# Kernel tuning notes

Measured on AMD Instinct MI355X. Metric: run time of the kernel, lower is better.

Reference implementation:

```python
import jax, jax.numpy as jnp
import numpy as np

B, N, D = 4, 2048, 512
H = 8
HD = D // H
MLP_H = 4 * D
SCALE = HD ** -0.5
ELEV_SCALE = 1000.0
EPS = 1e-5


def _ln(x, g, b):
    m = jnp.mean(x, axis=-1, keepdims=True)
    v = jnp.mean((x - m) ** 2, axis=-1, keepdims=True)
    return (x - m) * jax.lax.rsqrt(v + EPS) * g + b


def setup_inputs() -> dict:
    key = jax.random.key(0)
    ks = jax.random.split(key, 10)
    s = lambda fin: (2.0 / fin) ** 0.5
    return {
        "x": jax.random.normal(ks[0], (B, N, D), jnp.float32),
        "elevation_patches": jax.random.uniform(ks[1], (B, N), jnp.float32) * 3000.0,
        "ln1_g": jnp.ones((D,), jnp.float32),
        "ln1_b": jnp.zeros((D,), jnp.float32),
        "qkv_w": jax.random.normal(ks[2], (D, 3 * D), jnp.float32) * s(D),
        "alpha": jnp.ones((1,), jnp.float32),
        "proj_w": jax.random.normal(ks[3], (D, D), jnp.float32) * s(D),
        "proj_b": jnp.zeros((D,), jnp.float32),
        "ln2_g": jnp.ones((D,), jnp.float32),
        "ln2_b": jnp.zeros((D,), jnp.float32),
        "fc1_w": jax.random.normal(ks[4], (D, MLP_H), jnp.float32) * s(D),
        "fc1_b": jnp.zeros((MLP_H,), jnp.float32),
        "fc2_w": jax.random.normal(ks[5], (MLP_H, D), jnp.float32) * s(MLP_H),
        "fc2_b": jnp.zeros((D,), jnp.float32),
    }


def reference(x, elevation_patches, ln1_g, ln1_b, qkv_w, alpha, proj_w, proj_b,
              ln2_g, ln2_b, fc1_w, fc1_b, fc2_w, fc2_b):
    # --- attention ---
    h = _ln(x, ln1_g, ln1_b)
    qkv = (h @ qkv_w).reshape(B, N, 3, H, HD)
    q, k, v = (jnp.moveaxis(qkv[:, :, i], 1, 2) for i in range(3))  # [B,H,N,HD]
    scores = jnp.einsum('bhnd,bhmd->bhnm', q, k) * SCALE
    elev_diff = (elevation_patches[:, None, :] - elevation_patches[:, :, None]) / ELEV_SCALE
    bias = jnp.clip(-alpha[0] * jax.nn.relu(elev_diff), -10.0, 0.0)  # [B,N,N]
    attn = jax.nn.softmax(scores + bias[:, None], axis=-1)
    out = jnp.einsum('bhnm,bhmd->bhnd', attn, v)
    out = jnp.moveaxis(out, 1, 2).reshape(B, N, D) @ proj_w + proj_b
    x = x + out
    # --- mlp ---
    h2 = _ln(x, ln2_g, ln2_b)
    mlp = jax.nn.gelu(h2 @ fc1_w + fc1_b, approximate=False) @ fc2_w + fc2_b
    return x + mlp
```

## Files before the change

### kernel.cpp

```cpp
#include <hip/hip_runtime.h>
#include <math.h>

typedef unsigned short u16;
typedef unsigned int u32;

#define B_ 4
#define N_ 2048
#define D_ 512
#define H_ 8
#define HD_ 64
#define MLP_H_ 2048
#define EPS_ 1e-5f
#define C2_ 14.426950408889634f
#define QSCALE_ 0.1803368801111204f
#define EL2_ 0.0014426950408889634f

#if __has_builtin(__builtin_amdgcn_exp2f)
#define EXP2(x) __builtin_amdgcn_exp2f(x)
#else
#define EXP2(x) exp2f(x)
#endif
#if __has_builtin(__builtin_amdgcn_fmed3f)
#define CLAMP0C(x) __builtin_amdgcn_fmed3f((x), 0.0f, C2_)
#else
#define CLAMP0C(x) fminf(fmaxf((x), 0.0f), C2_)
#endif

__device__ __forceinline__ u16 bf16_rne(float x) {
  u32 u = __float_as_uint(x);
  u32 r = (u + 0x7FFFu + ((u >> 16) & 1u)) >> 16;
  return (u16)r;
}
#if __has_builtin(__builtin_amdgcn_cvt_pk_bf16_f32)
typedef __bf16 bf2_t __attribute__((ext_vector_type(2)));
__device__ __forceinline__ u32 pk_bf16(float a, float b) {
  bf2_t v = __builtin_amdgcn_cvt_pk_bf16_f32(a, b);
  u32 r; __builtin_memcpy(&r, &v, 4); return r;
}
#else
__device__ __forceinline__ u32 pk_bf16(float a, float b) {
  return (u32)bf16_rne(a) | ((u32)bf16_rne(b) << 16);
}
#endif
__device__ __forceinline__ void bf16_split(float x, u16& h, u16& l) {
  h = bf16_rne(x);
  float hf = __uint_as_float(((u32)h) << 16);
  l = bf16_rne(x - hf);
}

typedef __attribute__((ext_vector_type(8))) short bfrag;
typedef __attribute__((ext_vector_type(4))) float ffrag;

#define LDS_AS(p) ((__attribute__((address_space(3))) void*)(p))
#define GLB_AS(p) ((const __attribute__((address_space(1))) void*)(p))

__global__ __launch_bounds__(256) void ln_kernel(
    const float* __restrict__ x, const float* __restrict__ g,
    const float* __restrict__ b, u16* __restrict__ o,
    const float* __restrict__ elev, const float* __restrict__ alpha,
    float* __restrict__ e2)
{
  __shared__ float red[8];
  int row = blockIdx.x;
  int tid = threadIdx.x;
  if (e2 && tid == 0) e2[row] = elev[row] * (alpha[0] * EL2_);
  const float* xr = x + (size_t)row * D_;
  float v0 = xr[tid], v1 = xr[tid + 256];
  float s = v0 + v1;
  #pragma unroll
  for (int off = 32; off > 0; off >>= 1) s += __shfl_xor(s, off, 64);
  if ((tid & 63) == 0) red[tid >> 6] = s;
  __syncthreads();
  float mean = (red[0] + red[1] + red[2] + red[3]) * (1.0f / D_);
  float d0 = v0 - mean, d1 = v1 - mean;
  float vs = d0 * d0 + d1 * d1;
  #pragma unroll
  for (int off = 32; off > 0; off >>= 1) vs += __shfl_xor(vs, off, 64);
  if ((tid & 63) == 0) red[4 + (tid >> 6)] = vs;
  __syncthreads();
  float var = (red[4] + red[5] + red[6] + red[7]) * (1.0f / D_);
  float r = rsqrtf(var + EPS_);
  u16* orow = o + (size_t)row * D_;
  orow[tid]       = bf16_rne(d0 * r * g[tid] + b[tid]);
  orow[tid + 256] = bf16_rne(d1 * r * g[tid + 256] + b[tid + 256]);
}

__device__ __forceinline__ void wsplit_body(
    const float* __restrict__ W, u16* __restrict__ Thi, u16* __restrict__ Tlo,
    int K, int N, int bx, int by, int tid)
{
  __shared__ float tile[64][65];
  int n0 = bx * 64, k0 = by * 64;
  int c = tid & 63, r4 = tid >> 6;
  #pragma unroll
  for (int i = 0; i < 16; i++) {
    int r = r4 + i * 4;
    tile[r][c] = W[(size_t)(k0 + r) * N + n0 + c];
  }
  __syncthreads();
  #pragma unroll
  for (int i = 0; i < 16; i++) {
    int rn = r4 + i * 4;
    float v = tile[c][rn];
    size_t o = (size_t)(n0 + rn) * K + k0 + c;
    if (Tlo) {
      u16 h, l; bf16_split(v, h, l);
      Thi[o] = h; Tlo[o] = l;
    } else {
      Thi[o] = bf16_rne(v);
    }
  }
}

__global__ __launch_bounds__(256) void wsplit_all(
    const float* __restrict__ qkv_w, const float* __restrict__ proj_w,
    const float* __restrict__ fc1_w, const float* __restrict__ fc2_w,
    u16* __restrict__ qw_hi, u16* __restrict__ qw_lo,
    u16* __restrict__ pw_hi, u16* __restrict__ f1_hi, u16* __restrict__ f2_hi)
{
  int id = blockIdx.x;
  int tid = threadIdx.x;
  if (id < 192) {
    wsplit_body(qkv_w, qw_hi, qw_lo, 512, 1536, id % 24, id / 24, tid);
  } else if (id < 256) {
    int l = id - 192;
    wsplit_body(proj_w, pw_hi, nullptr, 512, 512, l % 8, l / 8, tid);
  } else if (id < 512) {
    int l = id - 256;
    wsplit_body(fc1_w, f1_hi, nullptr, 512, 2048, l % 32, l / 32, tid);
  } else {
    int l = id - 512;
    wsplit_body(fc2_w, f2_hi, nullptr, 2048, 512, l % 8, l / 8, tid);
  }
}

template<int ROWS>
__device__ __forceinline__ void stage32(const u16* __restrict__ src, int ld,
                                        int r0, int k0, u16* lds, int lane, int wave)
{
  #pragma unroll
  for (int i = 0; i < ROWS / 64; i++) {
    int seg = wave * (ROWS / 64) + i;
    int chunk = seg * 64 + lane;
    int r = chunk >> 2;
    int c = (chunk & 3) ^ ((r >> 1) & 3);
    const u16* g = src + (size_t)(r0 + r) * ld + k0 + c * 8;
    __builtin_amdgcn_global_load_lds(GLB_AS(g), LDS_AS((char*)lds + seg * 1024), 16, 0, 0);
  }
}

__device__ __forceinline__ int swz_off(int R, int quad) {
  return R * 32 + ((quad ^ ((R >> 1) & 3)) * 8);
}

__global__ __launch_bounds__(256) void qkv_gemm(
    const u16* __restrict__ Ahi,
    const u16* __restrict__ Whi, const u16* __restrict__ Wlo,
    u16* __restrict__ qkh, u16* __restrict__ qkl, u16* __restrict__ vth)
{
  __shared__ __align__(16) u16 As0[128 * 32], As1[128 * 32];
  __shared__ __align__(16) u16 Bh0[64 * 32],  Bh1[64 * 32];
  __shared__ __align__(16) u16 Bl0[64 * 32],  Bl1[64 * 32];

  int tid = threadIdx.x;
  int lane = tid & 63, wave = tid >> 6;
  int ln = lane & 15, quad = lane >> 4;
  int m0 = blockIdx.y * 128, n0 = blockIdx.x * 64;
  bool lo = (n0 < 1024);

  ffrag acc[2][4] = {};

  for (int k0 = 0; k0 < D_; k0 += 64) {
    stage32<128>(Ahi, D_, m0, k0,      As0, lane, wave);
    stage32<128>(Ahi, D_, m0, k0 + 32, As1, lane, wave);
    stage32<64>(Whi, D_, n0, k0,      Bh0, lane, wave);
    stage32<64>(Whi, D_, n0, k0 + 32, Bh1, lane, wave);
    if (lo) {
      stage32<64>(Wlo, D_, n0, k0,      Bl0, lane, wave);
      stage32<64>(Wlo, D_, n0, k0 + 32, Bl1, lane, wave);
    }
    __syncthreads();

    #pragma unroll
    for (int hf = 0; hf < 2; hf++) {
      const u16* Asf = hf ? As1 : As0;
      const u16* Bhf = hf ? Bh1 : Bh0;
      const u16* Blf = hf ? Bl1 : Bl0;
      bfrag ah[2], bh[4], bl[4];
      #pragma unroll
      for (int t = 0; t < 2; t++)
        ah[t] = *(const bfrag*)(Asf + swz_off(wave * 32 + t * 16 + ln, quad));
      #pragma unroll
      for (int u = 0; u < 4; u++) {
        int off = swz_off(u * 16 + ln, quad);
        bh[u] = *(const bfrag*)(Bhf + off);
        bl[u] = *(const bfrag*)(Blf + off);
      }
      #pragma unroll
      for (int ti = 0; ti < 2; ti++) {
        #pragma unroll
        for (int tj = 0; tj < 4; tj++) {
          acc[ti][tj] = __builtin_amdgcn_mfma_f32_16x16x32_bf16(ah[ti], bh[tj], acc[ti][tj], 0, 0, 0);
          if (lo)
            acc[ti][tj] = __builtin_amdgcn_mfma_f32_16x16x32_bf16(ah[ti], bl[tj], acc[ti][tj], 0, 0, 0);
        }
      }
    }
    __syncthreads();
  }

  #pragma unroll
  for (int tj = 0; tj < 4; tj++) {
    int col = n0 + tj * 16 + ln;
    #pragma unroll
    for (int ti = 0; ti < 2; ti++) {
      int rw = m0 + wave * 32 + ti * 16 + quad * 4;
      if (col < 512) {
        #pragma unroll
        for (int r = 0; r < 4; r++) {
          float y = acc[ti][tj][r] * QSCALE_;
          u16 hh, ll; bf16_split(y, hh, ll);
          qkh[(size_t)(rw + r) * 1024 + col] = hh;
          qkl[(size_t)(rw + r) * 1024 + col] = ll;
        }
      } else if (col < 1024) {
        #pragma unroll
        for (int r = 0; r < 4; r++)
          qkh[(size_t)(rw + r) * 1024 + col] = bf16_rne(acc[ti][tj][r]);
      } else {
        int h = (col - 1024) >> 6, d = (col - 1024) & 63;
        int bb = rw >> 11, n = rw & (N_ - 1);
        u32 w0 = pk_bf16(acc[ti][tj][0], acc[ti][tj][1]);
        u32 w1 = pk_bf16(acc[ti][tj][2], acc[ti][tj][3]);
        size_t dst = ((size_t)((bb * H_ + h) * HD_ + d)) * N_ + n;
        *(uint2*)(vth + dst) = make_uint2(w0, w1);
      }
    }
  }
}

template<int TBM, int TBN, int WR, int WC>
__global__ __launch_bounds__(256) void gemm_tpl(
    const u16* __restrict__ Ahi, const u16* __restrict__ Whi,
    const float* __restrict__ bias, const float* __restrict__ res,
    float* __restrict__ Cf, u16* __restrict__ Ohi,
    int M, int K, int N, int act)
{
  constexpr int MF = TBM / (WR * 16);
  constexpr int NF = TBN / (WC * 16);
  constexpr int AT = TBM * 32;
  constexpr int BT = TBN * 32;
  __shared__ __align__(16) u16 smem[2 * AT + 2 * BT];
  u16* As0 = smem;          u16* As1 = smem + AT;
  u16* Bh0 = smem + 2 * AT; u16* Bh1 = smem + 2 * AT + BT;

  int tid = threadIdx.x;
  int lane = tid & 63, wave = tid >> 6;
  int wr = wave / WC, wc = wave % WC;
  int ln = lane & 15, quad = lane >> 4;
  int m0 = blockIdx.y * TBM, n0 = blockIdx.x * TBN;

  ffrag acc[MF][NF] = {};

  for (int k0 = 0; k0 < K; k0 += 64) {
    stage32<TBM>(Ahi, K, m0, k0,      As0, lane, wave);
    stage32<TBM>(Ahi, K, m0, k0 + 32, As1, lane, wave);
    stage32<TBN>(Whi, K, n0, k0,      Bh0, lane, wave);
    stage32<TBN>(Whi, K, n0, k0 + 32, Bh1, lane, wave);
    __syncthreads();

    #pragma unroll
    for (int hf = 0; hf < 2; hf++) {
      const u16* Asf = hf ? As1 : As0;
      const u16* Bhf = hf ? Bh1 : Bh0;
      bfrag ah[MF], bh[NF];
      #pragma unroll
      for (int t = 0; t < MF; t++)
        ah[t] = *(const bfrag*)(Asf + swz_off(wr * (TBM / WR) + t * 16 + ln, quad));
      #pragma unroll
      for (int u = 0; u < NF; u++)
        bh[u] = *(const bfrag*)(Bhf + swz_off(wc * (TBN / WC) + u * 16 + ln, quad));
      #pragma unroll
      for (int ti = 0; ti < MF; ti++)
        #pragma unroll
        for (int tj = 0; tj < NF; tj++)
          acc[ti][tj] = __builtin_amdgcn_mfma_f32_16x16x32_bf16(ah[ti], bh[tj], acc[ti][tj], 0, 0, 0);
    }
    __syncthreads();
  }

  #pragma unroll
  for (int tj = 0; tj < NF; tj++) {
    int col = n0 + wc * (TBN / WC) + tj * 16 + ln;
    float bv = bias ? bias[col] : 0.f;
    #pragma unroll
    for (int ti = 0; ti < MF; ti++) {
      int rw = m0 + wr * (TBM / WR) + ti * 16 + quad * 4;
      #pragma unroll
      for (int r = 0; r < 4; r++) {
        float y = acc[ti][tj][r] + bv;
        if (act) y = 0.5f * y * (1.f + erff(y * 0.70710678118654752f));
        if (res) y += res[(size_t)(rw + r) * N + col];
        if (Cf) Cf[(size_t)(rw + r) * N + col] = y;
        if (Ohi) Ohi[(size_t)(rw + r) * N + col] = bf16_rne(y);
      }
    }
  }
}

__device__ __forceinline__ void stage_tile64(const u16* __restrict__ gbase, size_t rstride,
                                             u16* lds, int wave, int lane)
{
  #pragma unroll
  for (int i = 0; i < 2; i++) {
    int seg = wave * 2 + i;
    int chunk = seg * 64 + lane;
    int ch = chunk >> 8;
    int pc = chunk & 255;
    int r = pc >> 2;
    int q = (pc & 3) ^ ((r >> 1) & 3);
    const u16* g = gbase + (size_t)r * rstride + ch * 32 + q * 8;
    __builtin_amdgcn_global_load_lds(GLB_AS(g), LDS_AS((char*)lds + seg * 1024), 16, 0, 0);
  }
}

__device__ __forceinline__ int frag_off(int c, int R, int quad) {
  return c * 2048 + R * 32 + ((quad ^ ((R >> 1) & 3)) * 8);
}

__global__ __launch_bounds__(256) void attn_mfma_kernel(
    const u16* __restrict__ qkh, const u16* __restrict__ qkl,
    const u16* __restrict__ vth,
    const float* __restrict__ e2, u16* __restrict__ outb)
{
  __shared__ __align__(16) u16 Kh[2][4096];
  __shared__ __align__(16) u16 Vh[2][4096];
  __shared__ __align__(16) u16 Pw[4][16][72];

  int b = blockIdx.z, h = blockIdx.y;
  int q0 = blockIdx.x * 64;
  int tid = threadIdx.x;
  int lane = tid & 63, wq = tid >> 6;
  int ln = lane & 15, quad = lane >> 4;

  const u16* qb_h = qkh + ((size_t)(b * N_ + q0)) * 1024 + h * 64;
  const u16* qb_l = qkl + ((size_t)(b * N_ + q0)) * 1024 + h * 64;
  stage_tile64(qb_h, 1024, Kh[0], wq, lane);
  stage_tile64(qb_l, 1024, Vh[0], wq, lane);
  __syncthreads();

  bfrag qfh[2], qfl[2];
  #pragma unroll
  for (int c = 0; c < 2; c++) {
    int off = frag_off(c, wq * 16 + ln, quad);
    qfh[c] = *(const bfrag*)(Kh[0] + off);
    qfl[c] = *(const bfrag*)(Vh[0] + off);
  }
  __syncthreads();

  float e2q = e2[b * N_ + q0 + wq * 16 + ln];
  float m_i = -3.0e38f, l_i = 0.f;
  ffrag O[4] = {};

  const u16* kp = qkh + (size_t)b * N_ * 1024 + 512 + h * 64;
  const u16* vp = vth + (size_t)(b * H_ + h) * HD_ * N_;
  const float* ep = e2 + b * N_;

  stage_tile64(kp, 1024, Kh[0], wq, lane);
  stage_tile64(vp, N_, Vh[0], wq, lane);
  kp += (size_t)64 * 1024;
  vp += 64;
  __syncthreads();

  for (int it = 0; it < N_ / 64; it++) {
    int cur = it & 1;
    if (it < N_ / 64 - 1) {
      stage_tile64(kp, 1024, Kh[cur ^ 1], wq, lane);
      stage_tile64(vp, N_, Vh[cur ^ 1], wq, lane);
      kp += (size_t)64 * 1024;
      vp += 64;
    }

    ffrag S[4];
    #pragma unroll
    for (int kt = 0; kt < 4; kt++) {
      ffrag s = {0.f, 0.f, 0.f, 0.f};
      #pragma unroll
      for (int c = 0; c < 2; c++) {
        bfrag kf = *(const bfrag*)(Kh[cur] + frag_off(c, kt * 16 + ln, quad));
        s = __builtin_amdgcn_mfma_f32_16x16x32_bf16(kf, qfh[c], s, 0, 0, 0);
        s = __builtin_amdgcn_mfma_f32_16x16x32_bf16(kf, qfl[c], s, 0, 0, 0);
      }
      S[kt] = s;
    }

    float4 ek[4];
    #pragma unroll
    for (int kt = 0; kt < 4; kt++)
      ek[kt] = *(const float4*)&ep[it * 64 + kt * 16 + quad * 4];

    float p[4][4];
    float mx = -3.0e38f;
    #pragma unroll
    for (int kt = 0; kt < 4; kt++) {
      #pragma unroll
      for (int r = 0; r < 4; r++) {
        float d = CLAMP0C((&ek[kt].x)[r] - e2q);
        float sv = S[kt][r] - d;
        p[kt][r] = sv;
        mx = fmaxf(mx, sv);
      }
    }
    mx = fmaxf(mx, __shfl_xor(mx, 16, 64));
    mx = fmaxf(mx, __shfl_xor(mx, 32, 64));
    float mnew = fmaxf(m_i, mx);
    float corr = EXP2(m_i - mnew);
    float ps = 0.f;
    #pragma unroll
    for (int kt = 0; kt < 4; kt++) {
      #pragma unroll
      for (int r = 0; r < 4; r++) {
        float pv = EXP2(p[kt][r] - mnew);
        p[kt][r] = pv;
        ps += pv;
      }
    }
    ps += __shfl_xor(ps, 16, 64);
    ps += __shfl_xor(ps, 32, 64);
    m_i = mnew;
    l_i = l_i * corr + ps;
    #pragma unroll
    for (int dt = 0; dt < 4; dt++) O[dt] *= corr;

    #pragma unroll
    for (int kt = 0; kt < 4; kt++) {
      u32 w0 = pk_bf16(p[kt][0], p[kt][1]);
      u32 w1 = pk_bf16(p[kt][2], p[kt][3]);
      *(uint2*)&Pw[wq][ln][kt * 16 + quad * 4] = make_uint2(w0, w1);
    }

    bfrag pf[2];
    #pragma unroll
    for (int c = 0; c < 2; c++)
      pf[c] = *(const bfrag*)&Pw[wq][ln][c * 32 + quad * 8];

    #pragma unroll
    for (int dt = 0; dt < 4; dt++) {
      ffrag o = O[dt];
      #pragma unroll
      for (int c = 0; c < 2; c++) {
        bfrag vf = *(const bfrag*)(Vh[cur] + frag_off(c, dt * 16 + ln, quad));
        o = __builtin_amdgcn_mfma_f32_16x16x32_bf16(vf, pf[c], o, 0, 0, 0);
      }
      O[dt] = o;
    }
    __syncthreads();
  }

  float inv = 1.0f / l_i;
  int row = q0 + wq * 16 + ln;
  #pragma unroll
  for (int dt = 0; dt < 4; dt++) {
    u32 w0 = pk_bf16(O[dt][0] * inv, O[dt][1] * inv);
    u32 w1 = pk_bf16(O[dt][2] * inv, O[dt][3] * inv);
    *(uint2*)&outb[((size_t)(b * N_ + row)) * D_ + h * 64 + dt * 16 + quad * 4] =
        make_uint2(w0, w1);
  }
}

extern "C" void kernel_launch(void* const* d_in, const int* in_sizes, int n_in,
                              void* d_out, int out_size, void* d_ws, size_t ws_size,
                              hipStream_t stream) {
  const float* x      = (const float*)d_in[0];
  const float* elev   = (const float*)d_in[1];
  const float* ln1_g  = (const float*)d_in[2];
  const float* ln1_b  = (const float*)d_in[3];
  const float* qkv_w  = (const float*)d_in[4];
  const float* alpha  = (const float*)d_in[5];
  const float* proj_w = (const float*)d_in[6];
  const float* proj_b = (const float*)d_in[7];
  const float* ln2_g  = (const float*)d_in[8];
  const float* ln2_b  = (const float*)d_in[9];
  const float* fc1_w  = (const float*)d_in[10];
  const float* fc1_b  = (const float*)d_in[11];
  const float* fc2_w  = (const float*)d_in[12];
  const float* fc2_b  = (const float*)d_in[13];
  float* out = (float*)d_out;

  const size_t HBf  = (size_t)B_ * N_ * D_;
  const size_t QKE  = (size_t)B_ * N_ * 1024;
  const size_t MLPE = (size_t)B_ * N_ * MLP_H_;

  char* p = (char*)d_ws;
  u16* abuf = (u16*)p;                     p += HBf * 2;
  char* region = p;                        p += MLPE * 2;
  u16* qkh    = (u16*)region;
  u16* qkl    = (u16*)(region + QKE * 2);
  u16* mlp_hi = (u16*)region;
  u16* vth  = (u16*)p;  p += HBf * 2;
  float* xres = (float*)p;                 p += HBf * 4;
  u16* qw_hi = (u16*)p;  p += (size_t)D_ * 3 * D_ * 2;
  u16* qw_lo = (u16*)p;  p += (size_t)D_ * 3 * D_ * 2;
  u16* pw_hi = (u16*)p;  p += (size_t)D_ * D_ * 2;
  u16* f1_hi = (u16*)p;  p += (size_t)D_ * MLP_H_ * 2;
  u16* f2_hi = (u16*)p;  p += (size_t)MLP_H_ * D_ * 2;
  float* e2  = (float*)p; p += (size_t)B_ * N_ * 4;

  const int rows = B_ * N_;

  wsplit_all<<<768, 256, 0, stream>>>(qkv_w, proj_w, fc1_w, fc2_w,
                                      qw_hi, qw_lo, pw_hi, f1_hi, f2_hi);
  ln_kernel<<<rows, 256, 0, stream>>>(x, ln1_g, ln1_b, abuf, elev, alpha, e2);
  qkv_gemm<<<dim3(1536 / 64, rows / 128), 256, 0, stream>>>(
      abuf, qw_hi, qw_lo, qkh, qkl, vth);
  attn_mfma_kernel<<<dim3(N_ / 64, H_, B_), 256, 0, stream>>>(
      qkh, qkl, vth, e2, abuf);
  gemm_tpl<64, 64, 2, 2><<<dim3(D_ / 64, rows / 64), 256, 0, stream>>>(
      abuf, pw_hi, proj_b, x, xres, nullptr, rows, D_, D_, 0);
  ln_kernel<<<rows, 256, 0, stream>>>(xres, ln2_g, ln2_b, abuf, nullptr, nullptr, nullptr);
  gemm_tpl<64, 128, 1, 4><<<dim3(MLP_H_ / 128, rows / 64), 256, 0, stream>>>(
      abuf, f1_hi, fc1_b, nullptr, nullptr, mlp_hi, rows, D_, MLP_H_, 1);
  gemm_tpl<64, 64, 2, 2><<<dim3(D_ / 64, rows / 64), 256, 0, stream>>>(
      mlp_hi, f2_hi, fc2_b, xres, out, nullptr, rows, MLP_H_, D_, 0);
}
```

Before: 356.3 us.

## Merge layernorm into prep kernel and single-buffer attention K/V tiles

```diff
diff --git a/kernel.cpp b/kernel.cpp
--- a/kernel.cpp
+++ b/kernel.cpp
@@ -54,16 +54,11 @@
 #define LDS_AS(p) ((__attribute__((address_space(3))) void*)(p))
 #define GLB_AS(p) ((const __attribute__((address_space(1))) void*)(p))
 
-__global__ __launch_bounds__(256) void ln_kernel(
+__device__ __forceinline__ void ln_body(
     const float* __restrict__ x, const float* __restrict__ g,
-    const float* __restrict__ b, u16* __restrict__ o,
-    const float* __restrict__ elev, const float* __restrict__ alpha,
-    float* __restrict__ e2)
+    const float* __restrict__ b, u16* __restrict__ o, int row, int tid)
 {
   __shared__ float red[8];
-  int row = blockIdx.x;
-  int tid = threadIdx.x;
-  if (e2 && tid == 0) e2[row] = elev[row] * (alpha[0] * EL2_);
   const float* xr = x + (size_t)row * D_;
   float v0 = xr[tid], v1 = xr[tid + 256];
   float s = v0 + v1;
@@ -83,6 +78,13 @@
   u16* orow = o + (size_t)row * D_;
   orow[tid]       = bf16_rne(d0 * r * g[tid] + b[tid]);
   orow[tid + 256] = bf16_rne(d1 * r * g[tid + 256] + b[tid + 256]);
+}
+
+__global__ __launch_bounds__(256) void ln_kernel(
+    const float* __restrict__ x, const float* __restrict__ g,
+    const float* __restrict__ b, u16* __restrict__ o)
+{
+  ln_body(x, g, b, o, blockIdx.x, threadIdx.x);
 }
 
 __device__ __forceinline__ void wsplit_body(
@@ -112,14 +114,24 @@
   }
 }
 
-__global__ __launch_bounds__(256) void wsplit_all(
+__global__ __launch_bounds__(256) void prep_kernel(
+    const float* __restrict__ x, const float* __restrict__ ln1_g,
+    const float* __restrict__ ln1_b, u16* __restrict__ abuf,
+    const float* __restrict__ elev, const float* __restrict__ alpha,
+    float* __restrict__ e2,
     const float* __restrict__ qkv_w, const float* __restrict__ proj_w,
     const float* __restrict__ fc1_w, const float* __restrict__ fc2_w,
     u16* __restrict__ qw_hi, u16* __restrict__ qw_lo,
     u16* __restrict__ pw_hi, u16* __restrict__ f1_hi, u16* __restrict__ f2_hi)
 {
-  int id = blockIdx.x;
+  int blk = blockIdx.x;
   int tid = threadIdx.x;
+  if (blk < 8192) {
+    if (tid == 0) e2[blk] = elev[blk] * (alpha[0] * EL2_);
+    ln_body(x, ln1_g, ln1_b, abuf, blk, tid);
+    return;
+  }
+  int id = blk - 8192;
   if (id < 192) {
     wsplit_body(qkv_w, qw_hi, qw_lo, 512, 1536, id % 24, id / 24, tid);
   } else if (id < 256) {
@@ -333,8 +345,8 @@
     const u16* __restrict__ vth,
     const float* __restrict__ e2, u16* __restrict__ outb)
 {
-  __shared__ __align__(16) u16 Kh[2][4096];
-  __shared__ __align__(16) u16 Vh[2][4096];
+  __shared__ __align__(16) u16 Kh[4096];
+  __shared__ __align__(16) u16 Vh[4096];
   __shared__ __align__(16) u16 Pw[4][16][72];
 
   int b = blockIdx.z, h = blockIdx.y;
@@ -345,16 +357,16 @@
 
   const u16* qb_h = qkh + ((size_t)(b * N_ + q0)) * 1024 + h * 64;
   const u16* qb_l = qkl + ((size_t)(b * N_ + q0)) * 1024 + h * 64;
-  stage_tile64(qb_h, 1024, Kh[0], wq, lane);
-  stage_tile64(qb_l, 1024, Vh[0], wq, lane);
+  stage_tile64(qb_h, 1024, Kh, wq, lane);
+  stage_tile64(qb_l, 1024, Vh, wq, lane);
   __syncthreads();
 
   bfrag qfh[2], qfl[2];
   #pragma unroll
   for (int c = 0; c < 2; c++) {
     int off = frag_off(c, wq * 16 + ln, quad);
-    qfh[c] = *(const bfrag*)(Kh[0] + off);
-    qfl[c] = *(const bfrag*)(Vh[0] + off);
+    qfh[c] = *(const bfrag*)(Kh + off);
+    qfl[c] = *(const bfrag*)(Vh + off);
   }
   __syncthreads();
 
@@ -366,20 +378,12 @@
   const u16* vp = vth + (size_t)(b * H_ + h) * HD_ * N_;
   const float* ep = e2 + b * N_;
 
-  stage_tile64(kp, 1024, Kh[0], wq, lane);
-  stage_tile64(vp, N_, Vh[0], wq, lane);
-  kp += (size_t)64 * 1024;
-  vp += 64;
-  __syncthreads();
-
-  for (int it = 0; it < N_ / 64; it++) {
-    int cur = it & 1;
-    if (it < N_ / 64 - 1) {
-      stage_tile64(kp, 1024, Kh[cur ^ 1], wq, lane);
-      stage_tile64(vp, N_, Vh[cur ^ 1], wq, lane);
-      kp += (size_t)64 * 1024;
-      vp += 64;
-    }
+  for (int k0 = 0; k0 < N_; k0 += 64) {
+    stage_tile64(kp, 1024, Kh, wq, lane);
+    stage_tile64(vp, N_, Vh, wq, lane);
+    kp += (size_t)64 * 1024;
+    vp += 64;
+    __syncthreads();
 
     ffrag S[4];
     #pragma unroll
@@ -387,7 +391,7 @@
       ffrag s = {0.f, 0.f, 0.f, 0.f};
       #pragma unroll
       for (int c = 0; c < 2; c++) {
-        bfrag kf = *(const bfrag*)(Kh[cur] + frag_off(c, kt * 16 + ln, quad));
+        bfrag kf = *(const bfrag*)(Kh + frag_off(c, kt * 16 + ln, quad));
         s = __builtin_amdgcn_mfma_f32_16x16x32_bf16(kf, qfh[c], s, 0, 0, 0);
         s = __builtin_amdgcn_mfma_f32_16x16x32_bf16(kf, qfl[c], s, 0, 0, 0);
       }
@@ -397,7 +401,7 @@
     float4 ek[4];
     #pragma unroll
     for (int kt = 0; kt < 4; kt++)
-      ek[kt] = *(const float4*)&ep[it * 64 + kt * 16 + quad * 4];
+      ek[kt] = *(const float4*)&ep[k0 + kt * 16 + quad * 4];
 
     float p[4][4];
     float mx = -3.0e38f;
@@ -449,7 +453,7 @@
       ffrag o = O[dt];
       #pragma unroll
       for (int c = 0; c < 2; c++) {
-        bfrag vf = *(const bfrag*)(Vh[cur] + frag_off(c, dt * 16 + ln, quad));
+        bfrag vf = *(const bfrag*)(Vh + frag_off(c, dt * 16 + ln, quad));
         o = __builtin_amdgcn_mfma_f32_16x16x32_bf16(vf, pf[c], o, 0, 0, 0);
       }
       O[dt] = o;
@@ -508,16 +512,16 @@
 
   const int rows = B_ * N_;
 
-  wsplit_all<<<768, 256, 0, stream>>>(qkv_w, proj_w, fc1_w, fc2_w,
-                                      qw_hi, qw_lo, pw_hi, f1_hi, f2_hi);
-  ln_kernel<<<rows, 256, 0, stream>>>(x, ln1_g, ln1_b, abuf, elev, alpha, e2);
+  prep_kernel<<<rows + 768, 256, 0, stream>>>(
+      x, ln1_g, ln1_b, abuf, elev, alpha, e2,
+      qkv_w, proj_w, fc1_w, fc2_w, qw_hi, qw_lo, pw_hi, f1_hi, f2_hi);
   qkv_gemm<<<dim3(1536 / 64, rows / 128), 256, 0, stream>>>(
       abuf, qw_hi, qw_lo, qkh, qkl, vth);
   attn_mfma_kernel<<<dim3(N_ / 64, H_, B_), 256, 0, stream>>>(
       qkh, qkl, vth, e2, abuf);
   gemm_tpl<64, 64, 2, 2><<<dim3(D_ / 64, rows / 64), 256, 0, stream>>>(
       abuf, pw_hi, proj_b, x, xres, nullptr, rows, D_, D_, 0);
-  ln_kernel<<<rows, 256, 0, stream>>>(xres, ln2_g, ln2_b, abuf, nullptr, nullptr, nullptr);
+  ln_kernel<<<rows, 256, 0, stream>>>(xres, ln2_g, ln2_b, abuf);
   gemm_tpl<64, 128, 1, 4><<<dim3(MLP_H_ / 128, rows / 64), 256, 0, stream>>>(
       abuf, f1_hi, fc1_b, nullptr, nullptr, mlp_hi, rows, D_, MLP_H_, 1);
   gemm_tpl<64, 64, 2, 2><<<dim3(D_ / 64, rows / 64), 256, 0, stream>>>(
```

Result: faster. 346.9 us (-2.6%).
